# Performance work log

Hardware: AMD Instinct MI355X
Metric: run time of the kernel (lower is better)

Reference implementation:

```python
import jax, jax.numpy as jnp
import numpy as np

NA, NS = 50000, 5000          # artist / style node counts
E_AA, E_AS = 500000, 250000   # edges per edge type
C, ED = 128, 8                # hidden dim, edge-attr dim
DIN_A, DIN_S = 128, 64        # input feature dims
NUM_LAYERS = 3


def _l2norm(x):
    # F.normalize(x, dim=-1): x / max(||x||_2, eps)
    n = jnp.sqrt(jnp.sum(x * x, axis=-1, keepdims=True))
    return x / jnp.maximum(n, 1e-12)


def _gatv2(x_src, x_dst, src, dst, eattr, Wl, Wr, att, We, b, num_dst):
    # PyG GATv2Conv, heads=1, concat=True, add_self_loops=False, edge_dim=ED
    xl = x_src @ Wl                      # [Nsrc, C] transformed source
    xr = x_dst @ Wr                      # [Ndst, C] transformed target
    m = xl[src] + xr[dst] + eattr @ We   # [E, C]
    e = jax.nn.leaky_relu(m, 0.2) @ att  # [E] attention logits
    # segment softmax over destination nodes
    emax = jax.ops.segment_max(e, dst, num_segments=num_dst)
    ee = jnp.exp(e - emax[dst])
    den = jax.ops.segment_sum(ee, dst, num_segments=num_dst)
    alpha = ee / jnp.maximum(den[dst], 1e-16)
    out = jax.ops.segment_sum(alpha[:, None] * xl[src], dst, num_segments=num_dst)
    return out + b


def setup_inputs() -> dict:
    key = jax.random.key(0)
    ks = iter(jax.random.split(key, 40))
    r = lambda shape, s=1.0: s * jax.random.normal(next(ks), shape, dtype=jnp.float32)
    d = {}
    d['x_artist'] = r((NA, DIN_A))
    d['x_style'] = r((NS, DIN_S))
    d['src_aa'] = jax.random.randint(next(ks), (E_AA,), 0, NA, dtype=jnp.int32)
    d['dst_aa'] = jax.random.randint(next(ks), (E_AA,), 0, NA, dtype=jnp.int32)
    d['eattr_aa'] = r((E_AA, ED))
    d['src_as'] = jax.random.randint(next(ks), (E_AS,), 0, NA, dtype=jnp.int32)
    d['dst_as'] = jax.random.randint(next(ks), (E_AS,), 0, NS, dtype=jnp.int32)
    d['eattr_as'] = r((E_AS, ED))
    w = 0.1
    # layer 0 (input dims differ per edge type)
    d['Wl0_aa'] = r((DIN_A, C), w); d['Wr0_aa'] = r((DIN_A, C), w)
    d['att0_aa'] = r((C,), w); d['We0_aa'] = r((ED, C), w); d['b0_aa'] = r((C,), w)
    d['Wl0_as'] = r((DIN_A, C), w); d['Wr0_as'] = r((DIN_S, C), w)
    d['att0_as'] = r((C,), w); d['We0_as'] = r((ED, C), w); d['b0_as'] = r((C,), w)
    # layers 1..2 stacked
    d['Wl_aa'] = r((2, C, C), w); d['Wr_aa'] = r((2, C, C), w)
    d['att_aa'] = r((2, C), w); d['We_aa'] = r((2, ED, C), w); d['b_aa'] = r((2, C), w)
    d['Wl_as'] = r((2, C, C), w); d['Wr_as'] = r((2, C, C), w)
    d['att_as'] = r((2, C), w); d['We_as'] = r((2, ED, C), w); d['b_as'] = r((2, C), w)
    return d


def reference(x_artist, x_style, src_aa, dst_aa, eattr_aa, src_as, dst_as, eattr_as,
              Wl0_aa, Wr0_aa, att0_aa, We0_aa, b0_aa,
              Wl0_as, Wr0_as, att0_as, We0_as, b0_as,
              Wl_aa, Wr_aa, att_aa, We_aa, b_aa,
              Wl_as, Wr_as, att_as, We_as, b_as):
    ha, hs = x_artist, x_style
    for i in range(NUM_LAYERS):
        if i == 0:
            p_aa = (Wl0_aa, Wr0_aa, att0_aa, We0_aa, b0_aa)
            p_as = (Wl0_as, Wr0_as, att0_as, We0_as, b0_as)
        else:
            j = i - 1
            p_aa = (Wl_aa[j], Wr_aa[j], att_aa[j], We_aa[j], b_aa[j])
            p_as = (Wl_as[j], Wr_as[j], att_as[j], We_as[j], b_as[j])
        # HeteroConv: each dst node type receives from exactly one edge type here
        na = _gatv2(ha, ha, src_aa, dst_aa, eattr_aa, *p_aa, NA)
        ns = _gatv2(ha, hs, src_as, dst_as, eattr_as, *p_as, NS)
        if i < NUM_LAYERS - 1:
            na = jax.nn.relu(na)
            ns = jax.nn.relu(ns)
        # dropout p=0.0 -> identity; then L2 normalize per node
        ha, hs = _l2norm(na), _l2norm(ns)
    return ha, hs
```

## Files before the change

kernel.cpp:

```cpp
#include <hip/hip_runtime.h>
#include <hip/hip_bf16.h>
#include <math.h>

#define NA 50000
#define NS 5000
#define E_AA 500000
#define E_AS 250000
#define CDIM 128
#define ED 8
#define NAPAD 50176
#define NSPAD 5120
#define SCAN_CH 2048
#define AGG_BLOCKS 1024

typedef __attribute__((ext_vector_type(8))) short bf16x8;
typedef __attribute__((ext_vector_type(4))) float f32x4;

__device__ inline short f2bf(float f) {
    __hip_bfloat16 h = __float2bfloat16(f);
    return *(short*)&h;
}
__device__ inline float bf2f(short s) {
    union { unsigned int u; float f; } cv;
    cv.u = ((unsigned int)(unsigned short)s) << 16;
    return cv.f;
}


__device__ inline float4 f4fma(float s, float4 a, float4 b) {
    return make_float4(fmaf(s, a.x, b.x), fmaf(s, a.y, b.y),
                       fmaf(s, a.z, b.z), fmaf(s, a.w, b.w));
}
__device__ inline float4 f4add(float4 a, float4 b) {
    return make_float4(a.x + b.x, a.y + b.y, a.z + b.z, a.w + b.w);
}
__device__ inline float4 f4leaky(float4 a) {
    return make_float4(a.x > 0.f ? a.x : 0.2f * a.x, a.y > 0.f ? a.y : 0.2f * a.y,
                       a.z > 0.f ? a.z : 0.2f * a.z, a.w > 0.f ? a.w : 0.2f * a.w);
}
__device__ inline float f4dot(float4 a, float4 b) {
    return a.x * b.x + a.y * b.y + a.z * b.z + a.w * b.w;
}
__device__ inline float4 f4mix(float sc, float4 a, float p, float4 x) {
    return make_float4(fmaf(sc, a.x, p * x.x), fmaf(sc, a.y, p * x.y),
                       fmaf(sc, a.z, p * x.z), fmaf(sc, a.w, p * x.w));
}
__device__ inline float4 bfh2f4(bf16x8 v, int half) {
    int o = half * 4;
    return make_float4(bf2f(v[o]), bf2f(v[o + 1]), bf2f(v[o + 2]), bf2f(v[o + 3]));
}


__global__ __launch_bounds__(256) void count2_k(const int* __restrict__ dst0,
                                                const int* __restrict__ dst1,
                                                int* __restrict__ deg0,
                                                int* __restrict__ deg1) {
    int e = blockIdx.x * 256 + threadIdx.x;
    if (e < E_AA) atomicAdd(&deg0[dst0[e]], 1);
    if (e < E_AS) atomicAdd(&deg1[dst1[e]], 1);
}

__global__ __launch_bounds__(256) void scanA_k(const int* __restrict__ deg0, int n0,
                                               const int* __restrict__ deg1, int n1,
                                               int nb0, int* __restrict__ bsum) {
    int b = blockIdx.x;
    const int* deg; int n; int lb;
    if ((int)b < nb0) { deg = deg0; n = n0; lb = b; }
    else { deg = deg1; n = n1; lb = b - nb0; }
    int t = threadIdx.x;
    int base = lb * SCAN_CH + t * 8;
    int s = 0;
    #pragma unroll
    for (int i = 0; i < 8; ++i) { int idx = base + i; s += (idx < n) ? deg[idx] : 0; }
    int lane = t & 63, w = t >> 6;
    #pragma unroll
    for (int off = 1; off < 64; off <<= 1) {
        int u = __shfl_up(s, off, 64);
        if (lane >= off) s += u;
    }
    __shared__ int ws[4];
    if (lane == 63) ws[w] = s;
    __syncthreads();
    if (t == 0) bsum[blockIdx.x] = ws[0] + ws[1] + ws[2] + ws[3];
}

__global__ void scanB_k(int* __restrict__ bsum, int nb0, int nb1) {
    int t = threadIdx.x;
    int n = nb0 + nb1;
    int v = (t < n) ? bsum[t] : 0;
    int incl = v;
    #pragma unroll
    for (int off = 1; off < 64; off <<= 1) {
        int u = __shfl_up(incl, off, 64);
        if (t >= off) incl += u;
    }
    int excl = incl - v;
    int sum0 = __shfl(incl, nb0 - 1, 64);
    if (t >= nb0) excl -= sum0;
    if (t < n) bsum[t] = excl;
}

__global__ __launch_bounds__(256) void scanC_k(const int* __restrict__ deg0, int n0,
                                               const int* __restrict__ deg1, int n1,
                                               int nb0, const int* __restrict__ bsum,
                                               int* __restrict__ rs0, int* __restrict__ rs1) {
    int b = blockIdx.x;
    const int* deg; int n; int* rs; int lb;
    if ((int)b < nb0) { deg = deg0; n = n0; rs = rs0; lb = b; }
    else { deg = deg1; n = n1; rs = rs1; lb = b - nb0; }
    int boff = bsum[b];
    int t = threadIdx.x;
    int base = lb * SCAN_CH + t * 8;
    int v[8];
    int tsum = 0;
    #pragma unroll
    for (int i = 0; i < 8; ++i) {
        int idx = base + i;
        v[i] = (idx < n) ? deg[idx] : 0;
        tsum += v[i];
    }
    int lane = t & 63, w = t >> 6;
    int incl = tsum;
    #pragma unroll
    for (int off = 1; off < 64; off <<= 1) {
        int u = __shfl_up(incl, off, 64);
        if (lane >= off) incl += u;
    }
    __shared__ int ws[4];
    if (lane == 63) ws[w] = incl;
    __syncthreads();
    int woff = 0;
    for (int i = 0; i < w; ++i) woff += ws[i];
    int run = boff + woff + incl - tsum;
    #pragma unroll
    for (int i = 0; i < 8; ++i) {
        int idx = base + i;
        if (idx < n) {
            rs[idx] = run;
            run += v[i];
            if (idx == n - 1) rs[n] = run;
        }
    }
}

__global__ __launch_bounds__(256) void scatter2_k(
    const int* __restrict__ dst0, const int* __restrict__ src0, const float* __restrict__ ea0,
    const int* __restrict__ dst1, const int* __restrict__ src1, const float* __restrict__ ea1,
    const int* __restrict__ rs0, const int* __restrict__ rs1,
    int* __restrict__ cur0, int* __restrict__ cur1,
    int* __restrict__ csrsrc0, int* __restrict__ csrsrc1,
    short* __restrict__ eas0, short* __restrict__ eas1) {
    int e = blockIdx.x * 256 + threadIdx.x;
    if (e < E_AA) {
        int d = dst0[e];
        int pos = atomicAdd(&cur0[d], 1);
        int slot = rs0[d] + pos;
        csrsrc0[slot] = src0[e];
        float4 a = ((const float4*)ea0)[(size_t)e * 2];
        float4 b = ((const float4*)ea0)[(size_t)e * 2 + 1];
        bf16x8 pk;
        pk[0] = f2bf(a.x); pk[1] = f2bf(a.y); pk[2] = f2bf(a.z); pk[3] = f2bf(a.w);
        pk[4] = f2bf(b.x); pk[5] = f2bf(b.y); pk[6] = f2bf(b.z); pk[7] = f2bf(b.w);
        *(bf16x8*)(eas0 + (size_t)slot * 8) = pk;
    }
    if (e < E_AS) {
        int d = dst1[e];
        int pos = atomicAdd(&cur1[d], 1);
        int slot = rs1[d] + pos;
        csrsrc1[slot] = src1[e];
        float4 a = ((const float4*)ea1)[(size_t)e * 2];
        float4 b = ((const float4*)ea1)[(size_t)e * 2 + 1];
        bf16x8 pk;
        pk[0] = f2bf(a.x); pk[1] = f2bf(a.y); pk[2] = f2bf(a.z); pk[3] = f2bf(a.w);
        pk[4] = f2bf(b.x); pk[5] = f2bf(b.y); pk[6] = f2bf(b.z); pk[7] = f2bf(b.w);
        *(bf16x8*)(eas1 + (size_t)slot * 8) = pk;
    }
}


__global__ __launch_bounds__(256) void deghist2_k(const int* __restrict__ rs0, int n0,
                                                  const int* __restrict__ rs1, int n1,
                                                  int nb0, int* __restrict__ dh0,
                                                  int* __restrict__ dh1) {
    int b = blockIdx.x;
    const int* rs; int n; int* dh; int lb;
    if ((int)b < nb0) { rs = rs0; n = n0; dh = dh0; lb = b; }
    else { rs = rs1; n = n1; dh = dh1; lb = b - nb0; }
    __shared__ int lh[256];
    int t = threadIdx.x;
    lh[t] = 0;
    __syncthreads();
    int d = lb * 256 + t;
    if (d < n) {
        int deg = rs[d + 1] - rs[d];
        if (deg > 255) deg = 255;
        atomicAdd(&lh[deg], 1);
    }
    __syncthreads();
    if (lh[t]) atomicAdd(&dh[t], lh[t]);
}

__global__ void binscan2_k(const int* __restrict__ dh0, const int* __restrict__ dh1,
                           int* __restrict__ dbo0, int* __restrict__ dbo1) {
    int w = threadIdx.x >> 6, lane = threadIdx.x & 63;
    const int* dh = w ? dh1 : dh0;
    int* dbo = w ? dbo1 : dbo0;
    int v[4]; int s = 0;
    #pragma unroll
    for (int i = 0; i < 4; ++i) { v[i] = dh[lane * 4 + i]; s += v[i]; }
    int incl = s;
    #pragma unroll
    for (int off = 1; off < 64; off <<= 1) {
        int u = __shfl_up(incl, off, 64);
        if (lane >= off) incl += u;
    }
    int run = incl - s;
    #pragma unroll
    for (int i = 0; i < 4; ++i) { dbo[lane * 4 + i] = run; run += v[i]; }
}

__global__ __launch_bounds__(256) void degscatter2_k(const int* __restrict__ rs0, int n0,
                                                     const int* __restrict__ rs1, int n1,
                                                     int nb0,
                                                     const int* __restrict__ dbo0,
                                                     const int* __restrict__ dbo1,
                                                     int* __restrict__ dcur0,
                                                     int* __restrict__ dcur1,
                                                     int4* __restrict__ jobs0,
                                                     int4* __restrict__ jobs1) {
    int b = blockIdx.x;
    const int* rs; int n; const int* dbo; int* dcur; int4* jobs; int lb;
    if ((int)b < nb0) { rs = rs0; n = n0; dbo = dbo0; dcur = dcur0; jobs = jobs0; lb = b; }
    else { rs = rs1; n = n1; dbo = dbo1; dcur = dcur1; jobs = jobs1; lb = b - nb0; }
    __shared__ int lh[256];
    __shared__ int lbase[256];
    int t = threadIdx.x;
    lh[t] = 0;
    __syncthreads();
    int d = lb * 256 + t;
    int deg = 0, lpos = 0, e0 = 0, degc = 0;
    if (d < n) {
        e0 = rs[d];
        deg = rs[d + 1] - e0;
        degc = deg > 255 ? 255 : deg;
        lpos = atomicAdd(&lh[degc], 1);
    }
    __syncthreads();
    int cnt = lh[t];
    if (cnt) lbase[t] = atomicAdd(&dcur[t], cnt);
    __syncthreads();
    if (d < n) jobs[dbo[degc] + lbase[degc] + lpos] = make_int4(d, e0, deg, 0);
}


__global__ __launch_bounds__(256) void cvt2_k(const float* __restrict__ xa,
                                              const float* __restrict__ xs,
                                              short* __restrict__ Xb,
                                              short* __restrict__ Xsb) {
    const int t4A = NAPAD * 32;
    const int t4S = NSPAD * 32;
    int i = blockIdx.x * 256 + threadIdx.x;
    if (i < t4A) {
        int row = i >> 5, c4 = i & 31;
        float4 v = make_float4(0.f, 0.f, 0.f, 0.f);
        if (row < NA) v = ((const float4*)xa)[(size_t)row * 32 + c4];
        short4 s;
        s.x = f2bf(v.x); s.y = f2bf(v.y); s.z = f2bf(v.z); s.w = f2bf(v.w);
        ((short4*)Xb)[i] = s;
    } else if (i < t4A + t4S) {
        int j = i - t4A;
        int row = j >> 5, c4 = j & 31;
        float4 v = make_float4(0.f, 0.f, 0.f, 0.f);
        if (row < NS && c4 < 16) v = ((const float4*)xs)[(size_t)row * 16 + c4];
        short4 s;
        s.x = f2bf(v.x); s.y = f2bf(v.y); s.z = f2bf(v.z); s.w = f2bf(v.w);
        ((short4*)Xsb)[j] = s;
    }
}


__global__ __launch_bounds__(256) void wtr12_k(
    const float* __restrict__ Wl0_aa, const float* __restrict__ Wr0_aa,
    const float* __restrict__ Wl0_as, const float* __restrict__ Wr0_as,
    const float* __restrict__ Wl_aa, const float* __restrict__ Wr_aa,
    const float* __restrict__ Wl_as, const float* __restrict__ Wr_as,
    short* __restrict__ Wt) {
    int mat = blockIdx.x >> 6;
    int layer = mat >> 2, w = mat & 3;
    int idx = (blockIdx.x & 63) * 256 + threadIdx.x;
    int k = idx >> 7, n = idx & 127;
    const float* W;
    int K = 128;
    if (layer == 0) {
        W = (w == 0) ? Wl0_aa : (w == 1) ? Wr0_aa : (w == 2) ? Wl0_as : Wr0_as;
        if (w == 3) K = 64;
    } else {
        int j = layer - 1;
        W = ((w == 0) ? Wl_aa : (w == 1) ? Wr_aa : (w == 2) ? Wl_as : Wr_as)
            + (size_t)j * 16384;
    }
    float v = (k < K) ? W[(size_t)k * 128 + n] : 0.f;
    Wt[(size_t)mat * 16384 + n * 128 + k] = f2bf(v);
}


__global__ __launch_bounds__(256) void gemm4_k(
    const short* __restrict__ Xb, const short* __restrict__ Xsb,
    const short* __restrict__ Wt,
    short* __restrict__ Y0b, short* __restrict__ Y1b, short* __restrict__ Y2b,
    short* __restrict__ Y3b, int gM) {
    int t = threadIdx.x;
    int wave = t >> 6, lane = t & 63;
    int quad = lane >> 4, l16 = lane & 15;
    bool style = (int)blockIdx.x >= gM;
    int rblk = style ? (int)blockIdx.x - gM : (int)blockIdx.x;
    const short* X = style ? Xsb : Xb;
    int rbase = rblk * 256 + wave * 64;

    bf16x8 a[4][4];
    #pragma unroll
    for (int rt = 0; rt < 4; ++rt) {
        const short* arow = X + (size_t)(rbase + rt * 16 + l16) * 128 + quad * 8;
        #pragma unroll
        for (int kb = 0; kb < 4; ++kb) a[rt][kb] = *(const bf16x8*)(arow + kb * 32);
    }

    if (!style) {
        short* Yp[3] = {Y0b, Y1b, Y2b};
        #pragma unroll
        for (int w = 0; w < 3; ++w) {
            const short* Wb = Wt + (size_t)w * 16384;
            #pragma unroll 2
            for (int nt = 0; nt < 8; ++nt) {
                const short* brow = Wb + (size_t)(nt * 16 + l16) * 128 + quad * 8;
                bf16x8 b[4];
                #pragma unroll
                for (int kb = 0; kb < 4; ++kb) b[kb] = *(const bf16x8*)(brow + kb * 32);
                f32x4 acc[4] = {{0,0,0,0},{0,0,0,0},{0,0,0,0},{0,0,0,0}};
                #pragma unroll
                for (int kb = 0; kb < 4; ++kb)
                    #pragma unroll
                    for (int rt = 0; rt < 4; ++rt)
                        acc[rt] = __builtin_amdgcn_mfma_f32_16x16x32_bf16(a[rt][kb], b[kb],
                                                                          acc[rt], 0, 0, 0);
                int col = nt * 16 + l16;
                #pragma unroll
                for (int rt = 0; rt < 4; ++rt) {
                    #pragma unroll
                    for (int r = 0; r < 4; ++r) {
                        int row = rbase + rt * 16 + quad * 4 + r;
                        if (row < NA) Yp[w][(size_t)row * 128 + col] = f2bf(acc[rt][r]);
                    }
                }
            }
        }
    } else {
        const short* Wb = Wt + (size_t)3 * 16384;
        #pragma unroll 2
        for (int nt = 0; nt < 8; ++nt) {
            const short* brow = Wb + (size_t)(nt * 16 + l16) * 128 + quad * 8;
            bf16x8 b[4];
            #pragma unroll
            for (int kb = 0; kb < 4; ++kb) b[kb] = *(const bf16x8*)(brow + kb * 32);
            f32x4 acc[4] = {{0,0,0,0},{0,0,0,0},{0,0,0,0},{0,0,0,0}};
            #pragma unroll
            for (int kb = 0; kb < 4; ++kb)
                #pragma unroll
                for (int rt = 0; rt < 4; ++rt)
                    acc[rt] = __builtin_amdgcn_mfma_f32_16x16x32_bf16(a[rt][kb], b[kb],
                                                                      acc[rt], 0, 0, 0);
            int col = nt * 16 + l16;
            #pragma unroll
            for (int rt = 0; rt < 4; ++rt) {
                #pragma unroll
                for (int r = 0; r < 4; ++r) {
                    int row = rbase + rt * 16 + quad * 4 + r;
                    if (row < NS) Y3b[(size_t)row * 128 + col] = f2bf(acc[rt][r]);
                }
            }
        }
    }
}


template<bool RELU>
__global__ __launch_bounds__(256, 2) void agg2_k(
    const short* __restrict__ xl0, const short* __restrict__ xr0,
    const short* __restrict__ eas0, const int* __restrict__ csrsrc0,
    const float* __restrict__ We0, const float* __restrict__ att0,
    const float* __restrict__ bias0, const int4* __restrict__ jobs0,
    float* __restrict__ out0, short* __restrict__ outb0, int nd0, int nblk0,
    const short* __restrict__ xl1, const short* __restrict__ xr1,
    const short* __restrict__ eas1, const int* __restrict__ csrsrc1,
    const float* __restrict__ We1, const float* __restrict__ att1,
    const float* __restrict__ bias1, const int4* __restrict__ jobs1,
    float* __restrict__ out1, short* __restrict__ outb1, int nd1, int nblk1) {

    int wave = threadIdx.x >> 6;
    int lane = threadIdx.x & 63;
    int g = lane >> 4;
    int sl = lane & 15;
    int c = sl * 8;
    int stride = gridDim.x;

    for (int seg = 0; seg < 2; ++seg) {
        const short* xl = seg ? xl1 : xl0;
        const short* xrp = seg ? xr1 : xr0;
        const short* eas = seg ? eas1 : eas0;
        const int* csrsrc = seg ? csrsrc1 : csrsrc0;
        const float* We = seg ? We1 : We0;
        const float* att = seg ? att1 : att0;
        const float* bias = seg ? bias1 : bias0;
        const int4* jobs = seg ? jobs1 : jobs0;
        float* out = seg ? out1 : out0;
        short* outb = seg ? outb1 : outb0;
        int ndst = seg ? nd1 : nd0;
        int nblk = seg ? nblk1 : nblk0;

        int blk = blockIdx.x;
        if (blk >= nblk) continue;

        float4 WeA[8], WeB[8];
        #pragma unroll
        for (int k = 0; k < 8; ++k) {
            WeA[k] = *(const float4*)(We + k * 128 + c);
            WeB[k] = *(const float4*)(We + k * 128 + c + 4);
        }
        float4 attA = *(const float4*)(att + c);
        float4 attB = *(const float4*)(att + c + 4);
        float4 bA = *(const float4*)(bias + c);
        float4 bB = *(const float4*)(bias + c + 4);
        #pragma unroll
        for (int k = 0; k < 8; ++k) {
            asm volatile("" : "+v"(WeA[k].x), "+v"(WeA[k].y), "+v"(WeA[k].z), "+v"(WeA[k].w));
            asm volatile("" : "+v"(WeB[k].x), "+v"(WeB[k].y), "+v"(WeB[k].z), "+v"(WeB[k].w));
        }
        asm volatile("" : "+v"(attA.x), "+v"(attA.y), "+v"(attA.z), "+v"(attA.w));
        asm volatile("" : "+v"(attB.x), "+v"(attB.y), "+v"(attB.z), "+v"(attB.w));

        auto load_job = [&](int b) -> int4 {
            int di = b * 16 + wave * 4 + g;
            bool h = di < ndst;
            int4 j = jobs[h ? (ndst - 1 - di) : 0];
            if (!h) j.z = 0;
            return j;
        };

        int4 jb = load_job(blk);
        bf16x8 xrb = *(const bf16x8*)(xrp + (size_t)jb.x * 128 + c);

        for (; blk < nblk; blk += stride) {
            int nb = blk + stride;
            int4 jbN = (nb < nblk) ? load_job(nb) : make_int4(0, 0, 0, 0);

            int d = jb.x, e0 = jb.y, cnt = jb.z;
            int di = blk * 16 + wave * 4 + g;
            bool has = di < ndst;
            float4 xrA = bfh2f4(xrb, 0), xrB = bfh2f4(xrb, 1);

            float4 accA = {0,0,0,0}, accB = {0,0,0,0};
            float den = 0.f, mrun = -INFINITY;
            int last = (cnt > 0) ? e0 + cnt - 1 : 0;

            int mc = cnt;
            mc = max(mc, __shfl_xor(mc, 16, 64));
            mc = max(mc, __shfl_xor(mc, 32, 64));
            int niter = (mc + 3) >> 2;

            auto lds_idx = [&](int ib, int* s) {
                #pragma unroll
                for (int j = 0; j < 4; ++j) {
                    int cj = (ib + j < last) ? ib + j : last;
                    s[j] = csrsrc[cj];
                }
            };
            auto lds_ea = [&](int ib, bf16x8* ea) {
                #pragma unroll
                for (int j = 0; j < 4; ++j) {
                    int cj = (ib + j < last) ? ib + j : last;
                    ea[j] = *(const bf16x8*)(eas + (size_t)cj * 8);
                }
            };
            auto lds_x = [&](const int* s, bf16x8* xb) {
                #pragma unroll
                for (int j = 0; j < 4; ++j)
                    xb[j] = *(const bf16x8*)(xl + (size_t)s[j] * 128 + c);
            };

            int sA[4], sB[4];
            bf16x8 xbA[4], xbB[4], eaA[4], eaB[4];

            if (niter > 0) {
                int st[4];
                lds_idx(e0, st);
                lds_ea(e0, eaA);
                lds_x(st, xbA);
                lds_idx(e0 + 4, sA);
            }

            auto step = [&](int i, bf16x8 (&xbC)[4], bf16x8 (&eaC)[4], int (&sNx)[4],
                            bf16x8 (&xbN)[4], bf16x8 (&eaN)[4], int (&sN2)[4]) {
                lds_x(sNx, xbN);
                lds_ea(e0 + i + 4, eaN);
                lds_idx(e0 + i + 8, sN2);

                float4 x0A = bfh2f4(xbC[0], 0), x0B = bfh2f4(xbC[0], 1);
                float4 x1A = bfh2f4(xbC[1], 0), x1B = bfh2f4(xbC[1], 1);
                float4 x2A = bfh2f4(xbC[2], 0), x2B = bfh2f4(xbC[2], 1);
                float4 x3A = bfh2f4(xbC[3], 0), x3B = bfh2f4(xbC[3], 1);

                auto logit = [&](float4 xA, float4 xB, bf16x8 eab) -> float {
                    float4 ea = bfh2f4(eab, 0), eb = bfh2f4(eab, 1);
                    float4 mA = f4add(xA, xrA), mB = f4add(xB, xrB);
                    mA = f4fma(ea.x, WeA[0], mA); mB = f4fma(ea.x, WeB[0], mB);
                    mA = f4fma(ea.y, WeA[1], mA); mB = f4fma(ea.y, WeB[1], mB);
                    mA = f4fma(ea.z, WeA[2], mA); mB = f4fma(ea.z, WeB[2], mB);
                    mA = f4fma(ea.w, WeA[3], mA); mB = f4fma(ea.w, WeB[3], mB);
                    mA = f4fma(eb.x, WeA[4], mA); mB = f4fma(eb.x, WeB[4], mB);
                    mA = f4fma(eb.y, WeA[5], mA); mB = f4fma(eb.y, WeB[5], mB);
                    mA = f4fma(eb.z, WeA[6], mA); mB = f4fma(eb.z, WeB[6], mB);
                    mA = f4fma(eb.w, WeA[7], mA); mB = f4fma(eb.w, WeB[7], mB);
                    return f4dot(f4leaky(mA), attA) + f4dot(f4leaky(mB), attB);
                };

                float t0 = logit(x0A, x0B, eaC[0]);
                float t1 = logit(x1A, x1B, eaC[1]);
                float t2 = logit(x2A, x2B, eaC[2]);
                float t3 = logit(x3A, x3B, eaC[3]);
                #pragma unroll
                for (int off = 8; off; off >>= 1) {
                    t0 += __shfl_xor(t0, off, 64);
                    t1 += __shfl_xor(t1, off, 64);
                    t2 += __shfl_xor(t2, off, 64);
                    t3 += __shfl_xor(t3, off, 64);
                }
                if (i + 1 >= cnt) t1 = -INFINITY;
                if (i + 2 >= cnt) t2 = -INFINITY;
                if (i + 3 >= cnt) t3 = -INFINITY;

                if (i < cnt) {
                    float m4 = fmaxf(fmaxf(t0, t1), fmaxf(t2, t3));
                    float nm = fmaxf(mrun, m4);
                    float sc = __expf(mrun - nm);
                    float p0 = __expf(t0 - nm);
                    float p1 = __expf(t1 - nm);
                    float p2 = __expf(t2 - nm);
                    float p3 = __expf(t3 - nm);
                    den = den * sc + p0 + p1 + p2 + p3;
                    accA = f4mix(sc, accA, p0, x0A);
                    accA = f4fma(p1, x1A, accA);
                    accA = f4fma(p2, x2A, accA);
                    accA = f4fma(p3, x3A, accA);
                    accB = f4mix(sc, accB, p0, x0B);
                    accB = f4fma(p1, x1B, accB);
                    accB = f4fma(p2, x2B, accB);
                    accB = f4fma(p3, x3B, accB);
                    mrun = nm;
                }
            };

            int it = 0;
            for (; it + 1 < niter; it += 2) {
                step(it * 4,     xbA, eaA, sA, xbB, eaB, sB);
                step(it * 4 + 4, xbB, eaB, sB, xbA, eaA, sA);
            }
            if (it < niter)
                step(it * 4, xbA, eaA, sA, xbB, eaB, sB);

            float inv = 1.f / fmaxf(den, 1e-16f);
            float4 oA = make_float4(accA.x * inv + bA.x, accA.y * inv + bA.y,
                                    accA.z * inv + bA.z, accA.w * inv + bA.w);
            float4 oB = make_float4(accB.x * inv + bB.x, accB.y * inv + bB.y,
                                    accB.z * inv + bB.z, accB.w * inv + bB.w);
            if (RELU) {
                oA = make_float4(fmaxf(oA.x,0.f), fmaxf(oA.y,0.f),
                                 fmaxf(oA.z,0.f), fmaxf(oA.w,0.f));
                oB = make_float4(fmaxf(oB.x,0.f), fmaxf(oB.y,0.f),
                                 fmaxf(oB.z,0.f), fmaxf(oB.w,0.f));
            }
            float ss = f4dot(oA, oA) + f4dot(oB, oB);
            #pragma unroll
            for (int off = 8; off; off >>= 1) ss += __shfl_xor(ss, off, 64);
            float innv = 1.f / fmaxf(sqrtf(ss), 1e-12f);
            oA = make_float4(oA.x * innv, oA.y * innv, oA.z * innv, oA.w * innv);
            oB = make_float4(oB.x * innv, oB.y * innv, oB.z * innv, oB.w * innv);
            if (has) {
                if (out) {
                    float4* op = (float4*)(out + (size_t)d * 128 + c);
                    op[0] = oA;
                    op[1] = oB;
                }
                if (outb) {
                    bf16x8 pk;
                    pk[0] = f2bf(oA.x); pk[1] = f2bf(oA.y); pk[2] = f2bf(oA.z); pk[3] = f2bf(oA.w);
                    pk[4] = f2bf(oB.x); pk[5] = f2bf(oB.y); pk[6] = f2bf(oB.z); pk[7] = f2bf(oB.w);
                    *(bf16x8*)(outb + (size_t)d * 128 + c) = pk;
                }
            }

            bf16x8 xrbN = *(const bf16x8*)(xrp + (size_t)jbN.x * 128 + c);
            jb = jbN;
            xrb = xrbN;
        }
    }
}


extern "C" void kernel_launch(void* const* d_in, const int* in_sizes, int n_in,
                              void* d_out, int out_size, void* d_ws, size_t ws_size,
                              hipStream_t stream) {
    const float* x_artist = (const float*)d_in[0];
    const float* x_style  = (const float*)d_in[1];
    const int*   src_aa   = (const int*)d_in[2];
    const int*   dst_aa   = (const int*)d_in[3];
    const float* eattr_aa = (const float*)d_in[4];
    const int*   src_as   = (const int*)d_in[5];
    const int*   dst_as   = (const int*)d_in[6];
    const float* eattr_as = (const float*)d_in[7];
    const float* Wl0_aa = (const float*)d_in[8];
    const float* Wr0_aa = (const float*)d_in[9];
    const float* att0_aa = (const float*)d_in[10];
    const float* We0_aa = (const float*)d_in[11];
    const float* b0_aa = (const float*)d_in[12];
    const float* Wl0_as = (const float*)d_in[13];
    const float* Wr0_as = (const float*)d_in[14];
    const float* att0_as = (const float*)d_in[15];
    const float* We0_as = (const float*)d_in[16];
    const float* b0_as = (const float*)d_in[17];
    const float* Wl_aa = (const float*)d_in[18];
    const float* Wr_aa = (const float*)d_in[19];
    const float* att_aa = (const float*)d_in[20];
    const float* We_aa = (const float*)d_in[21];
    const float* b_aa = (const float*)d_in[22];
    const float* Wl_as = (const float*)d_in[23];
    const float* Wr_as = (const float*)d_in[24];
    const float* att_as = (const float*)d_in[25];
    const float* We_as = (const float*)d_in[26];
    const float* b_as = (const float*)d_in[27];

    float* out = (float*)d_out;

    short* Xb    = (short*)d_ws;
    short* Xsb   = Xb + (size_t)NAPAD * 128;
    short* Wt    = Xsb + (size_t)NSPAD * 128;
    short* bufAb = Wt + 12 * 16384;
    short* bufDb = bufAb + (size_t)NA * 128;
    short* bufBb = bufDb + (size_t)NA * 128;
    short* bufCb = bufBb + (size_t)NA * 128;
    short* easAA = bufCb + (size_t)NSPAD * 128;
    short* easAS = easAA + (size_t)E_AA * 8;
    int* ip = (int*)(easAS + (size_t)E_AS * 8);
    int* zbase  = ip;
    int* deg_aa = ip;            ip += NA;
    int* cur_aa = ip;            ip += NA;
    int* deg_as = ip;            ip += NS;
    int* cur_as = ip;            ip += NS;
    int* dh_aa  = ip;            ip += 256;
    int* dh_as  = ip;            ip += 256;
    int* dcur_aa = ip;           ip += 256;
    int* dcur_as = ip;           ip += 256;
    size_t zbytes = (size_t)(ip - zbase) * sizeof(int);
    int4* jobs_aa = (int4*)ip;   ip += 4 * NA;
    int4* jobs_as = (int4*)ip;   ip += 4 * NS;
    int* rs_aa  = ip;            ip += NA + 1;
    int* rs_as  = ip;            ip += NS + 1;
    int* csrsrc_aa = ip;         ip += E_AA;
    int* csrsrc_as = ip;         ip += E_AS;
    int* dbo_aa = ip;            ip += 256;
    int* dbo_as = ip;            ip += 256;
    int* bsum   = ip;            ip += 64;

    const int nbA_scan = (NA + SCAN_CH - 1) / SCAN_CH;
    const int nbS_scan = (NS + SCAN_CH - 1) / SCAN_CH;
    const int nbA_node = (NA + 255) / 256;
    const int nbS_node = (NS + 255) / 256;
    const int gE = (E_AA + 255) / 256;

    hipMemsetAsync(zbase, 0, zbytes, stream);
    count2_k<<<gE, 256, 0, stream>>>(dst_aa, dst_as, deg_aa, deg_as);
    scanA_k<<<nbA_scan + nbS_scan, 256, 0, stream>>>(deg_aa, NA, deg_as, NS, nbA_scan, bsum);
    scanB_k<<<1, 64, 0, stream>>>(bsum, nbA_scan, nbS_scan);
    scanC_k<<<nbA_scan + nbS_scan, 256, 0, stream>>>(deg_aa, NA, deg_as, NS, nbA_scan,
                                                     bsum, rs_aa, rs_as);
    scatter2_k<<<gE, 256, 0, stream>>>(dst_aa, src_aa, eattr_aa,
                                       dst_as, src_as, eattr_as,
                                       rs_aa, rs_as, cur_aa, cur_as,
                                       csrsrc_aa, csrsrc_as, easAA, easAS);
    deghist2_k<<<nbA_node + nbS_node, 256, 0, stream>>>(rs_aa, NA, rs_as, NS, nbA_node,
                                                        dh_aa, dh_as);
    binscan2_k<<<1, 128, 0, stream>>>(dh_aa, dh_as, dbo_aa, dbo_as);
    degscatter2_k<<<nbA_node + nbS_node, 256, 0, stream>>>(rs_aa, NA, rs_as, NS, nbA_node,
                                                           dbo_aa, dbo_as, dcur_aa, dcur_as,
                                                           jobs_aa, jobs_as);
    cvt2_k<<<(NAPAD * 32 + NSPAD * 32 + 255) / 256, 256, 0, stream>>>(x_artist, x_style,
                                                                      Xb, Xsb);
    wtr12_k<<<12 * 64, 256, 0, stream>>>(Wl0_aa, Wr0_aa, Wl0_as, Wr0_as,
                                         Wl_aa, Wr_aa, Wl_as, Wr_as, Wt);

    const int gM = NAPAD / 256;
    const int gS4 = NSPAD / 256;
    const int aggA = (NA + 15) / 16;
    const int aggS = (NS + 15) / 16;

    for (int layer = 0; layer < 3; ++layer) {
        int j = layer - 1;
        const float *patt_aa, *pWe_aa, *pb_aa, *patt_as, *pWe_as, *pb_as;
        if (layer == 0) {
            patt_aa = att0_aa; pWe_aa = We0_aa; pb_aa = b0_aa;
            patt_as = att0_as; pWe_as = We0_as; pb_as = b0_as;
        } else {
            patt_aa = att_aa + (size_t)j * CDIM;
            pWe_aa = We_aa + (size_t)j * ED * CDIM;
            pb_aa = b_aa + (size_t)j * CDIM;
            patt_as = att_as + (size_t)j * CDIM;
            pWe_as = We_as + (size_t)j * ED * CDIM;
            pb_as = b_as + (size_t)j * CDIM;
        }
        const short* pWt = Wt + (size_t)layer * 4 * 16384;
        float* hA_out = (layer == 2) ? out : nullptr;
        float* hS_out = (layer == 2) ? out + (size_t)NA * CDIM : nullptr;
        short* hA_outb = (layer == 2) ? nullptr : Xb;
        short* hS_outb = (layer == 2) ? nullptr : Xsb;

        gemm4_k<<<gM + gS4, 256, 0, stream>>>(Xb, Xsb, pWt, bufAb, bufBb, bufDb, bufCb, gM);

        if (layer < 2)
            agg2_k<true><<<AGG_BLOCKS, 256, 0, stream>>>(
                bufAb, bufBb, easAA, csrsrc_aa, pWe_aa, patt_aa, pb_aa,
                jobs_aa, hA_out, hA_outb, NA, aggA,
                bufDb, bufCb, easAS, csrsrc_as, pWe_as, patt_as, pb_as,
                jobs_as, hS_out, hS_outb, NS, aggS);
        else
            agg2_k<false><<<AGG_BLOCKS, 256, 0, stream>>>(
                bufAb, bufBb, easAA, csrsrc_aa, pWe_aa, patt_aa, pb_aa,
                jobs_aa, hA_out, hA_outb, NA, aggA,
                bufDb, bufCb, easAS, csrsrc_as, pWe_as, patt_as, pb_as,
                jobs_as, hS_out, hS_outb, NS, aggS);
    }
}
```

Before: 535.2 us.

## Split GEMM blocks per weight matrix and partition aggregation grid by edge type

The GEMM kernel now launches three blocks per row tile, one per weight matrix, instead of one block looping over three matrices. This triples parallelism for the artist projections, at the cost of reloading the A tile three times. The aggregation kernel no longer runs the two edge types one after another in every block. It statically gives 711 blocks to artist-artist and the rest to artist-style, so both proceed concurrently, but the fixed ratio risks load imbalance.

```diff
diff --git a/kernel.cpp b/kernel.cpp
--- a/kernel.cpp
+++ b/kernel.cpp
@@ -12,6 +12,7 @@
 #define NSPAD 5120
 #define SCAN_CH 2048
 #define AGG_BLOCKS 1024
+#define AGG_BLK_AA 711
 
 typedef __attribute__((ext_vector_type(8))) short bf16x8;
 typedef __attribute__((ext_vector_type(4))) float f32x4;
@@ -312,9 +313,12 @@
     int t = threadIdx.x;
     int wave = t >> 6, lane = t & 63;
     int quad = lane >> 4, l16 = lane & 15;
-    bool style = (int)blockIdx.x >= gM;
-    int rblk = style ? (int)blockIdx.x - gM : (int)blockIdx.x;
+    int gM3 = gM * 3;
+    bool style = (int)blockIdx.x >= gM3;
     const short* X = style ? Xsb : Xb;
+    int rblk, w;
+    if (style) { rblk = (int)blockIdx.x - gM3; w = 3; }
+    else { rblk = (int)blockIdx.x / 3; w = (int)blockIdx.x % 3; }
     int rbase = rblk * 256 + wave * 64;
 
     bf16x8 a[4][4];
@@ -325,58 +329,29 @@
         for (int kb = 0; kb < 4; ++kb) a[rt][kb] = *(const bf16x8*)(arow + kb * 32);
     }
 
-    if (!style) {
-        short* Yp[3] = {Y0b, Y1b, Y2b};
+    short* Y = style ? Y3b : (w == 0 ? Y0b : (w == 1 ? Y1b : Y2b));
+    int nlim = style ? NS : NA;
+    const short* Wb = Wt + (size_t)w * 16384;
+    #pragma unroll 2
+    for (int nt = 0; nt < 8; ++nt) {
+        const short* brow = Wb + (size_t)(nt * 16 + l16) * 128 + quad * 8;
+        bf16x8 b[4];
         #pragma unroll
-        for (int w = 0; w < 3; ++w) {
-            const short* Wb = Wt + (size_t)w * 16384;
-            #pragma unroll 2
-            for (int nt = 0; nt < 8; ++nt) {
-                const short* brow = Wb + (size_t)(nt * 16 + l16) * 128 + quad * 8;
-                bf16x8 b[4];
-                #pragma unroll
-                for (int kb = 0; kb < 4; ++kb) b[kb] = *(const bf16x8*)(brow + kb * 32);
-                f32x4 acc[4] = {{0,0,0,0},{0,0,0,0},{0,0,0,0},{0,0,0,0}};
-                #pragma unroll
-                for (int kb = 0; kb < 4; ++kb)
-                    #pragma unroll
-                    for (int rt = 0; rt < 4; ++rt)
-                        acc[rt] = __builtin_amdgcn_mfma_f32_16x16x32_bf16(a[rt][kb], b[kb],
-                                                                          acc[rt], 0, 0, 0);
-                int col = nt * 16 + l16;
-                #pragma unroll
-                for (int rt = 0; rt < 4; ++rt) {
-                    #pragma unroll
-                    for (int r = 0; r < 4; ++r) {
-                        int row = rbase + rt * 16 + quad * 4 + r;
-                        if (row < NA) Yp[w][(size_t)row * 128 + col] = f2bf(acc[rt][r]);
-                    }
-                }
-            }
-        }
-    } else {
-        const short* Wb = Wt + (size_t)3 * 16384;
-        #pragma unroll 2
-        for (int nt = 0; nt < 8; ++nt) {
-            const short* brow = Wb + (size_t)(nt * 16 + l16) * 128 + quad * 8;
-            bf16x8 b[4];
+        for (int kb = 0; kb < 4; ++kb) b[kb] = *(const bf16x8*)(brow + kb * 32);
+        f32x4 acc[4] = {{0,0,0,0},{0,0,0,0},{0,0,0,0},{0,0,0,0}};
+        #pragma unroll
+        for (int kb = 0; kb < 4; ++kb)
             #pragma unroll
-            for (int kb = 0; kb < 4; ++kb) b[kb] = *(const bf16x8*)(brow + kb * 32);
-            f32x4 acc[4] = {{0,0,0,0},{0,0,0,0},{0,0,0,0},{0,0,0,0}};
+            for (int rt = 0; rt < 4; ++rt)
+                acc[rt] = __builtin_amdgcn_mfma_f32_16x16x32_bf16(a[rt][kb], b[kb],
+                                                                  acc[rt], 0, 0, 0);
+        int col = nt * 16 + l16;
+        #pragma unroll
+        for (int rt = 0; rt < 4; ++rt) {
             #pragma unroll
-            for (int kb = 0; kb < 4; ++kb)
-                #pragma unroll
-                for (int rt = 0; rt < 4; ++rt)
-                    acc[rt] = __builtin_amdgcn_mfma_f32_16x16x32_bf16(a[rt][kb], b[kb],
-                                                                      acc[rt], 0, 0, 0);
-            int col = nt * 16 + l16;
-            #pragma unroll
-            for (int rt = 0; rt < 4; ++rt) {
-                #pragma unroll
-                for (int r = 0; r < 4; ++r) {
-                    int row = rbase + rt * 16 + quad * 4 + r;
-                    if (row < NS) Y3b[(size_t)row * 128 + col] = f2bf(acc[rt][r]);
-                }
+            for (int r = 0; r < 4; ++r) {
+                int row = rbase + rt * 16 + quad * 4 + r;
+                if (row < nlim) Y[(size_t)row * 128 + col] = f2bf(acc[rt][r]);
             }
         }
     }
@@ -394,214 +369,211 @@
     const short* __restrict__ eas1, const int* __restrict__ csrsrc1,
     const float* __restrict__ We1, const float* __restrict__ att1,
     const float* __restrict__ bias1, const int4* __restrict__ jobs1,
-    float* __restrict__ out1, short* __restrict__ outb1, int nd1, int nblk1) {
+    float* __restrict__ out1, short* __restrict__ outb1, int nd1, int nblk1,
+    int nblkB0) {
 
     int wave = threadIdx.x >> 6;
     int lane = threadIdx.x & 63;
     int g = lane >> 4;
     int sl = lane & 15;
     int c = sl * 8;
-    int stride = gridDim.x;
-
-    for (int seg = 0; seg < 2; ++seg) {
-        const short* xl = seg ? xl1 : xl0;
-        const short* xrp = seg ? xr1 : xr0;
-        const short* eas = seg ? eas1 : eas0;
-        const int* csrsrc = seg ? csrsrc1 : csrsrc0;
-        const float* We = seg ? We1 : We0;
-        const float* att = seg ? att1 : att0;
-        const float* bias = seg ? bias1 : bias0;
-        const int4* jobs = seg ? jobs1 : jobs0;
-        float* out = seg ? out1 : out0;
-        short* outb = seg ? outb1 : outb0;
-        int ndst = seg ? nd1 : nd0;
-        int nblk = seg ? nblk1 : nblk0;
-
-        int blk = blockIdx.x;
-        if (blk >= nblk) continue;
-
-        float4 WeA[8], WeB[8];
+
+    const short* xl; const short* xrp; const short* eas; const int* csrsrc;
+    const float* We; const float* att; const float* bias;
+    const int4* jobs;
+    float* out; short* outb; int ndst, nblk, blk, stride;
+    if ((int)blockIdx.x < nblkB0) {
+        xl = xl0; xrp = xr0; eas = eas0; csrsrc = csrsrc0; We = We0; att = att0; bias = bias0;
+        jobs = jobs0; out = out0; outb = outb0; ndst = nd0; nblk = nblk0;
+        blk = blockIdx.x; stride = nblkB0;
+    } else {
+        xl = xl1; xrp = xr1; eas = eas1; csrsrc = csrsrc1; We = We1; att = att1; bias = bias1;
+        jobs = jobs1; out = out1; outb = outb1; ndst = nd1; nblk = nblk1;
+        blk = blockIdx.x - nblkB0; stride = gridDim.x - nblkB0;
+    }
+    if (blk >= nblk) return;
+
+    float4 WeA[8], WeB[8];
+    #pragma unroll
+    for (int k = 0; k < 8; ++k) {
+        WeA[k] = *(const float4*)(We + k * 128 + c);
+        WeB[k] = *(const float4*)(We + k * 128 + c + 4);
+    }
+    float4 attA = *(const float4*)(att + c);
+    float4 attB = *(const float4*)(att + c + 4);
+    float4 bA = *(const float4*)(bias + c);
+    float4 bB = *(const float4*)(bias + c + 4);
+    #pragma unroll
+    for (int k = 0; k < 8; ++k) {
+        asm volatile("" : "+v"(WeA[k].x), "+v"(WeA[k].y), "+v"(WeA[k].z), "+v"(WeA[k].w));
+        asm volatile("" : "+v"(WeB[k].x), "+v"(WeB[k].y), "+v"(WeB[k].z), "+v"(WeB[k].w));
+    }
+    asm volatile("" : "+v"(attA.x), "+v"(attA.y), "+v"(attA.z), "+v"(attA.w));
+    asm volatile("" : "+v"(attB.x), "+v"(attB.y), "+v"(attB.z), "+v"(attB.w));
+
+    auto load_job = [&](int b) -> int4 {
+        int di = b * 16 + wave * 4 + g;
+        bool h = di < ndst;
+        int4 j = jobs[h ? (ndst - 1 - di) : 0];
+        if (!h) j.z = 0;
+        j.w = h ? 1 : 0;
+        return j;
+    };
+
+    int4 jb = load_job(blk);
+    bf16x8 xrb = *(const bf16x8*)(xrp + (size_t)jb.x * 128 + c);
+
+    for (; blk < nblk; blk += stride) {
+        int nb = blk + stride;
+        int4 jbN = (nb < nblk) ? load_job(nb) : make_int4(0, 0, 0, 0);
+
+        int d = jb.x, e0 = jb.y, cnt = jb.z;
+        bool has = jb.w != 0;
+        float4 xrA = bfh2f4(xrb, 0), xrB = bfh2f4(xrb, 1);
+
+        float4 accA = {0,0,0,0}, accB = {0,0,0,0};
+        float den = 0.f, mrun = -INFINITY;
+        int last = (cnt > 0) ? e0 + cnt - 1 : 0;
+
+        int mc = cnt;
+        mc = max(mc, __shfl_xor(mc, 16, 64));
+        mc = max(mc, __shfl_xor(mc, 32, 64));
+        int niter = (mc + 3) >> 2;
+
+        auto lds_idx = [&](int ib, int* s) {
+            #pragma unroll
+            for (int j = 0; j < 4; ++j) {
+                int cj = (ib + j < last) ? ib + j : last;
+                s[j] = csrsrc[cj];
+            }
+        };
+        auto lds_ea = [&](int ib, bf16x8* ea) {
+            #pragma unroll
+            for (int j = 0; j < 4; ++j) {
+                int cj = (ib + j < last) ? ib + j : last;
+                ea[j] = *(const bf16x8*)(eas + (size_t)cj * 8);
+            }
+        };
+        auto lds_x = [&](const int* s, bf16x8* xb) {
+            #pragma unroll
+            for (int j = 0; j < 4; ++j)
+                xb[j] = *(const bf16x8*)(xl + (size_t)s[j] * 128 + c);
+        };
+
+        int sA[4], sB[4];
+        bf16x8 xbA[4], xbB[4], eaA[4], eaB[4];
+
+        if (niter > 0) {
+            int st[4];
+            lds_idx(e0, st);
+            lds_ea(e0, eaA);
+            lds_x(st, xbA);
+            lds_idx(e0 + 4, sA);
+        }
+
+        auto step = [&](int i, bf16x8 (&xbC)[4], bf16x8 (&eaC)[4], int (&sNx)[4],
+                        bf16x8 (&xbN)[4], bf16x8 (&eaN)[4], int (&sN2)[4]) {
+            lds_x(sNx, xbN);
+            lds_ea(e0 + i + 4, eaN);
+            lds_idx(e0 + i + 8, sN2);
+
+            float4 x0A = bfh2f4(xbC[0], 0), x0B = bfh2f4(xbC[0], 1);
+            float4 x1A = bfh2f4(xbC[1], 0), x1B = bfh2f4(xbC[1], 1);
+            float4 x2A = bfh2f4(xbC[2], 0), x2B = bfh2f4(xbC[2], 1);
+            float4 x3A = bfh2f4(xbC[3], 0), x3B = bfh2f4(xbC[3], 1);
+
+            auto logit = [&](float4 xA, float4 xB, bf16x8 eab) -> float {
+                float4 ea = bfh2f4(eab, 0), eb = bfh2f4(eab, 1);
+                float4 mA = f4add(xA, xrA), mB = f4add(xB, xrB);
+                mA = f4fma(ea.x, WeA[0], mA); mB = f4fma(ea.x, WeB[0], mB);
+                mA = f4fma(ea.y, WeA[1], mA); mB = f4fma(ea.y, WeB[1], mB);
+                mA = f4fma(ea.z, WeA[2], mA); mB = f4fma(ea.z, WeB[2], mB);
+                mA = f4fma(ea.w, WeA[3], mA); mB = f4fma(ea.w, WeB[3], mB);
+                mA = f4fma(eb.x, WeA[4], mA); mB = f4fma(eb.x, WeB[4], mB);
+                mA = f4fma(eb.y, WeA[5], mA); mB = f4fma(eb.y, WeB[5], mB);
+                mA = f4fma(eb.z, WeA[6], mA); mB = f4fma(eb.z, WeB[6], mB);
+                mA = f4fma(eb.w, WeA[7], mA); mB = f4fma(eb.w, WeB[7], mB);
+                return f4dot(f4leaky(mA), attA) + f4dot(f4leaky(mB), attB);
+            };
+
+            float t0 = logit(x0A, x0B, eaC[0]);
+            float t1 = logit(x1A, x1B, eaC[1]);
+            float t2 = logit(x2A, x2B, eaC[2]);
+            float t3 = logit(x3A, x3B, eaC[3]);
+            #pragma unroll
+            for (int off = 8; off; off >>= 1) {
+                t0 += __shfl_xor(t0, off, 64);
+                t1 += __shfl_xor(t1, off, 64);
+                t2 += __shfl_xor(t2, off, 64);
+                t3 += __shfl_xor(t3, off, 64);
+            }
+            if (i + 1 >= cnt) t1 = -INFINITY;
+            if (i + 2 >= cnt) t2 = -INFINITY;
+            if (i + 3 >= cnt) t3 = -INFINITY;
+
+            if (i < cnt) {
+                float m4 = fmaxf(fmaxf(t0, t1), fmaxf(t2, t3));
+                float nm = fmaxf(mrun, m4);
+                float sc = __expf(mrun - nm);
+                float p0 = __expf(t0 - nm);
+                float p1 = __expf(t1 - nm);
+                float p2 = __expf(t2 - nm);
+                float p3 = __expf(t3 - nm);
+                den = den * sc + p0 + p1 + p2 + p3;
+                accA = f4mix(sc, accA, p0, x0A);
+                accA = f4fma(p1, x1A, accA);
+                accA = f4fma(p2, x2A, accA);
+                accA = f4fma(p3, x3A, accA);
+                accB = f4mix(sc, accB, p0, x0B);
+                accB = f4fma(p1, x1B, accB);
+                accB = f4fma(p2, x2B, accB);
+                accB = f4fma(p3, x3B, accB);
+                mrun = nm;
+            }
+        };
+
+        int it = 0;
+        for (; it + 1 < niter; it += 2) {
+            step(it * 4,     xbA, eaA, sA, xbB, eaB, sB);
+            step(it * 4 + 4, xbB, eaB, sB, xbA, eaA, sA);
+        }
+        if (it < niter)
+            step(it * 4, xbA, eaA, sA, xbB, eaB, sB);
+
+        float inv = 1.f / fmaxf(den, 1e-16f);
+        float4 oA = make_float4(accA.x * inv + bA.x, accA.y * inv + bA.y,
+                                accA.z * inv + bA.z, accA.w * inv + bA.w);
+        float4 oB = make_float4(accB.x * inv + bB.x, accB.y * inv + bB.y,
+                                accB.z * inv + bB.z, accB.w * inv + bB.w);
+        if (RELU) {
+            oA = make_float4(fmaxf(oA.x,0.f), fmaxf(oA.y,0.f),
+                             fmaxf(oA.z,0.f), fmaxf(oA.w,0.f));
+            oB = make_float4(fmaxf(oB.x,0.f), fmaxf(oB.y,0.f),
+                             fmaxf(oB.z,0.f), fmaxf(oB.w,0.f));
+        }
+        float ss = f4dot(oA, oA) + f4dot(oB, oB);
         #pragma unroll
-        for (int k = 0; k < 8; ++k) {
-            WeA[k] = *(const float4*)(We + k * 128 + c);
-            WeB[k] = *(const float4*)(We + k * 128 + c + 4);
+        for (int off = 8; off; off >>= 1) ss += __shfl_xor(ss, off, 64);
+        float innv = 1.f / fmaxf(sqrtf(ss), 1e-12f);
+        oA = make_float4(oA.x * innv, oA.y * innv, oA.z * innv, oA.w * innv);
+        oB = make_float4(oB.x * innv, oB.y * innv, oB.z * innv, oB.w * innv);
+        if (has) {
+            if (out) {
+                float4* op = (float4*)(out + (size_t)d * 128 + c);
+                op[0] = oA;
+                op[1] = oB;
+            }
+            if (outb) {
+                bf16x8 pk;
+                pk[0] = f2bf(oA.x); pk[1] = f2bf(oA.y); pk[2] = f2bf(oA.z); pk[3] = f2bf(oA.w);
+                pk[4] = f2bf(oB.x); pk[5] = f2bf(oB.y); pk[6] = f2bf(oB.z); pk[7] = f2bf(oB.w);
+                *(bf16x8*)(outb + (size_t)d * 128 + c) = pk;
+            }
         }
-        float4 attA = *(const float4*)(att + c);
-        float4 attB = *(const float4*)(att + c + 4);
-        float4 bA = *(const float4*)(bias + c);
-        float4 bB = *(const float4*)(bias + c + 4);
-        #pragma unroll
-        for (int k = 0; k < 8; ++k) {
-            asm volatile("" : "+v"(WeA[k].x), "+v"(WeA[k].y), "+v"(WeA[k].z), "+v"(WeA[k].w));
-            asm volatile("" : "+v"(WeB[k].x), "+v"(WeB[k].y), "+v"(WeB[k].z), "+v"(WeB[k].w));
-        }
-        asm volatile("" : "+v"(attA.x), "+v"(attA.y), "+v"(attA.z), "+v"(attA.w));
-        asm volatile("" : "+v"(attB.x), "+v"(attB.y), "+v"(attB.z), "+v"(attB.w));
-
-        auto load_job = [&](int b) -> int4 {
-            int di = b * 16 + wave * 4 + g;
-            bool h = di < ndst;
-            int4 j = jobs[h ? (ndst - 1 - di) : 0];
-            if (!h) j.z = 0;
-            return j;
-        };
-
-        int4 jb = load_job(blk);
-        bf16x8 xrb = *(const bf16x8*)(xrp + (size_t)jb.x * 128 + c);
-
-        for (; blk < nblk; blk += stride) {
-            int nb = blk + stride;
-            int4 jbN = (nb < nblk) ? load_job(nb) : make_int4(0, 0, 0, 0);
-
-            int d = jb.x, e0 = jb.y, cnt = jb.z;
-            int di = blk * 16 + wave * 4 + g;
-            bool has = di < ndst;
-            float4 xrA = bfh2f4(xrb, 0), xrB = bfh2f4(xrb, 1);
-
-            float4 accA = {0,0,0,0}, accB = {0,0,0,0};
-            float den = 0.f, mrun = -INFINITY;
-            int last = (cnt > 0) ? e0 + cnt - 1 : 0;
-
-            int mc = cnt;
-            mc = max(mc, __shfl_xor(mc, 16, 64));
-            mc = max(mc, __shfl_xor(mc, 32, 64));
-            int niter = (mc + 3) >> 2;
-
-            auto lds_idx = [&](int ib, int* s) {
-                #pragma unroll
-                for (int j = 0; j < 4; ++j) {
-                    int cj = (ib + j < last) ? ib + j : last;
-                    s[j] = csrsrc[cj];
-                }
-            };
-            auto lds_ea = [&](int ib, bf16x8* ea) {
-                #pragma unroll
-                for (int j = 0; j < 4; ++j) {
-                    int cj = (ib + j < last) ? ib + j : last;
-                    ea[j] = *(const bf16x8*)(eas + (size_t)cj * 8);
-                }
-            };
-            auto lds_x = [&](const int* s, bf16x8* xb) {
-                #pragma unroll
-                for (int j = 0; j < 4; ++j)
-                    xb[j] = *(const bf16x8*)(xl + (size_t)s[j] * 128 + c);
-            };
-
-            int sA[4], sB[4];
-            bf16x8 xbA[4], xbB[4], eaA[4], eaB[4];
-
-            if (niter > 0) {
-                int st[4];
-                lds_idx(e0, st);
-                lds_ea(e0, eaA);
-                lds_x(st, xbA);
-                lds_idx(e0 + 4, sA);
-            }
-
-            auto step = [&](int i, bf16x8 (&xbC)[4], bf16x8 (&eaC)[4], int (&sNx)[4],
-                            bf16x8 (&xbN)[4], bf16x8 (&eaN)[4], int (&sN2)[4]) {
-                lds_x(sNx, xbN);
-                lds_ea(e0 + i + 4, eaN);
-                lds_idx(e0 + i + 8, sN2);
-
-                float4 x0A = bfh2f4(xbC[0], 0), x0B = bfh2f4(xbC[0], 1);
-                float4 x1A = bfh2f4(xbC[1], 0), x1B = bfh2f4(xbC[1], 1);
-                float4 x2A = bfh2f4(xbC[2], 0), x2B = bfh2f4(xbC[2], 1);
-                float4 x3A = bfh2f4(xbC[3], 0), x3B = bfh2f4(xbC[3], 1);
-
-                auto logit = [&](float4 xA, float4 xB, bf16x8 eab) -> float {
-                    float4 ea = bfh2f4(eab, 0), eb = bfh2f4(eab, 1);
-                    float4 mA = f4add(xA, xrA), mB = f4add(xB, xrB);
-                    mA = f4fma(ea.x, WeA[0], mA); mB = f4fma(ea.x, WeB[0], mB);
-                    mA = f4fma(ea.y, WeA[1], mA); mB = f4fma(ea.y, WeB[1], mB);
-                    mA = f4fma(ea.z, WeA[2], mA); mB = f4fma(ea.z, WeB[2], mB);
-                    mA = f4fma(ea.w, WeA[3], mA); mB = f4fma(ea.w, WeB[3], mB);
-                    mA = f4fma(eb.x, WeA[4], mA); mB = f4fma(eb.x, WeB[4], mB);
-                    mA = f4fma(eb.y, WeA[5], mA); mB = f4fma(eb.y, WeB[5], mB);
-                    mA = f4fma(eb.z, WeA[6], mA); mB = f4fma(eb.z, WeB[6], mB);
-                    mA = f4fma(eb.w, WeA[7], mA); mB = f4fma(eb.w, WeB[7], mB);
-                    return f4dot(f4leaky(mA), attA) + f4dot(f4leaky(mB), attB);
-                };
-
-                float t0 = logit(x0A, x0B, eaC[0]);
-                float t1 = logit(x1A, x1B, eaC[1]);
-                float t2 = logit(x2A, x2B, eaC[2]);
-                float t3 = logit(x3A, x3B, eaC[3]);
-                #pragma unroll
-                for (int off = 8; off; off >>= 1) {
-                    t0 += __shfl_xor(t0, off, 64);
-                    t1 += __shfl_xor(t1, off, 64);
-                    t2 += __shfl_xor(t2, off, 64);
-                    t3 += __shfl_xor(t3, off, 64);
-                }
-                if (i + 1 >= cnt) t1 = -INFINITY;
-                if (i + 2 >= cnt) t2 = -INFINITY;
-                if (i + 3 >= cnt) t3 = -INFINITY;
-
-                if (i < cnt) {
-                    float m4 = fmaxf(fmaxf(t0, t1), fmaxf(t2, t3));
-                    float nm = fmaxf(mrun, m4);
-                    float sc = __expf(mrun - nm);
-                    float p0 = __expf(t0 - nm);
-                    float p1 = __expf(t1 - nm);
-                    float p2 = __expf(t2 - nm);
-                    float p3 = __expf(t3 - nm);
-                    den = den * sc + p0 + p1 + p2 + p3;
-                    accA = f4mix(sc, accA, p0, x0A);
-                    accA = f4fma(p1, x1A, accA);
-                    accA = f4fma(p2, x2A, accA);
-                    accA = f4fma(p3, x3A, accA);
-                    accB = f4mix(sc, accB, p0, x0B);
-                    accB = f4fma(p1, x1B, accB);
-                    accB = f4fma(p2, x2B, accB);
-                    accB = f4fma(p3, x3B, accB);
-                    mrun = nm;
-                }
-            };
-
-            int it = 0;
-            for (; it + 1 < niter; it += 2) {
-                step(it * 4,     xbA, eaA, sA, xbB, eaB, sB);
-                step(it * 4 + 4, xbB, eaB, sB, xbA, eaA, sA);
-            }
-            if (it < niter)
-                step(it * 4, xbA, eaA, sA, xbB, eaB, sB);
-
-            float inv = 1.f / fmaxf(den, 1e-16f);
-            float4 oA = make_float4(accA.x * inv + bA.x, accA.y * inv + bA.y,
-                                    accA.z * inv + bA.z, accA.w * inv + bA.w);
-            float4 oB = make_float4(accB.x * inv + bB.x, accB.y * inv + bB.y,
-                                    accB.z * inv + bB.z, accB.w * inv + bB.w);
-            if (RELU) {
-                oA = make_float4(fmaxf(oA.x,0.f), fmaxf(oA.y,0.f),
-                                 fmaxf(oA.z,0.f), fmaxf(oA.w,0.f));
-                oB = make_float4(fmaxf(oB.x,0.f), fmaxf(oB.y,0.f),
-                                 fmaxf(oB.z,0.f), fmaxf(oB.w,0.f));
-            }
-            float ss = f4dot(oA, oA) + f4dot(oB, oB);
-            #pragma unroll
-            for (int off = 8; off; off >>= 1) ss += __shfl_xor(ss, off, 64);
-            float innv = 1.f / fmaxf(sqrtf(ss), 1e-12f);
-            oA = make_float4(oA.x * innv, oA.y * innv, oA.z * innv, oA.w * innv);
-            oB = make_float4(oB.x * innv, oB.y * innv, oB.z * innv, oB.w * innv);
-            if (has) {
-                if (out) {
-                    float4* op = (float4*)(out + (size_t)d * 128 + c);
-                    op[0] = oA;
-                    op[1] = oB;
-                }
-                if (outb) {
-                    bf16x8 pk;
-                    pk[0] = f2bf(oA.x); pk[1] = f2bf(oA.y); pk[2] = f2bf(oA.z); pk[3] = f2bf(oA.w);
-                    pk[4] = f2bf(oB.x); pk[5] = f2bf(oB.y); pk[6] = f2bf(oB.z); pk[7] = f2bf(oB.w);
-                    *(bf16x8*)(outb + (size_t)d * 128 + c) = pk;
-                }
-            }
-
-            bf16x8 xrbN = *(const bf16x8*)(xrp + (size_t)jbN.x * 128 + c);
-            jb = jbN;
-            xrb = xrbN;
-        }
+
+        bf16x8 xrbN = *(const bf16x8*)(xrp + (size_t)jbN.x * 128 + c);
+        jb = jbN;
+        xrb = xrbN;
     }
 }
 
@@ -722,19 +694,19 @@
         short* hA_outb = (layer == 2) ? nullptr : Xb;
         short* hS_outb = (layer == 2) ? nullptr : Xsb;
 
-        gemm4_k<<<gM + gS4, 256, 0, stream>>>(Xb, Xsb, pWt, bufAb, bufBb, bufDb, bufCb, gM);
+        gemm4_k<<<3 * gM + gS4, 256, 0, stream>>>(Xb, Xsb, pWt, bufAb, bufBb, bufDb, bufCb, gM);
 
         if (layer < 2)
             agg2_k<true><<<AGG_BLOCKS, 256, 0, stream>>>(
                 bufAb, bufBb, easAA, csrsrc_aa, pWe_aa, patt_aa, pb_aa,
                 jobs_aa, hA_out, hA_outb, NA, aggA,
                 bufDb, bufCb, easAS, csrsrc_as, pWe_as, patt_as, pb_as,
-                jobs_as, hS_out, hS_outb, NS, aggS);
+                jobs_as, hS_out, hS_outb, NS, aggS, AGG_BLK_AA);
         else
             agg2_k<false><<<AGG_BLOCKS, 256, 0, stream>>>(
                 bufAb, bufBb, easAA, csrsrc_aa, pWe_aa, patt_aa, pb_aa,
                 jobs_aa, hA_out, hA_outb, NA, aggA,
                 bufDb, bufCb, easAS, csrsrc_as, pWe_as, patt_as, pb_as,
-                jobs_as, hS_out, hS_outb, NS, aggS);
-    }
-}
+                jobs_as, hS_out, hS_outb, NS, aggS, AGG_BLK_AA);
+    }
+}
```

New measurement: 507.2 us. 1.06x faster.
